# Optimization experiments

Hardware: AMD Instinct MI355X
Metric: run time of the kernel (lower is better)

## Reference

```python
import jax, jax.numpy as jnp
import numpy as np

EPS = 1e-5

def rmsnorm(x, w):
    var = jnp.mean(x * x, axis=-1, keepdims=True)
    return x * jax.lax.rsqrt(var + EPS) * w

def apply_rope(x, cos, sin):
    # x: [B, S, H, D], cos/sin: [S, D//2]; llama-style complex rotation over pairs
    B, S, H, D = x.shape
    xr = x.reshape(B, S, H, D // 2, 2)
    x0, x1 = xr[..., 0], xr[..., 1]
    c = cos[None, :, None, :]
    s = sin[None, :, None, :]
    o0 = x0 * c - x1 * s
    o1 = x0 * s + x1 * c
    return jnp.stack([o0, o1], axis=-1).reshape(B, S, H, D)

def setup_inputs() -> dict:
    key = jax.random.key(0)
    ks = jax.random.split(key, 8)
    B, S, dim = 2, 2048, 2048
    H, nope, rope = 16, 128, 64
    q_lr, kv_lr = 1536, 512
    hd = nope + rope
    x = jax.random.normal(ks[0], (B, S, dim), jnp.float32)
    wd_q = jax.random.normal(ks[1], (dim, q_lr), jnp.float32) * (dim ** -0.5)
    wu_q = jax.random.normal(ks[2], (q_lr, H * hd), jnp.float32) * (q_lr ** -0.5)
    q_norm_w = jnp.ones((q_lr,), jnp.float32)
    wd_kv = jax.random.normal(ks[3], (dim, kv_lr + rope), jnp.float32) * (dim ** -0.5)
    wu_kv = jax.random.normal(ks[4], (kv_lr, H * 2 * nope), jnp.float32) * (kv_lr ** -0.5)
    kv_norm_w = jnp.ones((kv_lr,), jnp.float32)
    wo = jax.random.normal(ks[5], (H * nope, dim), jnp.float32) * ((H * nope) ** -0.5)
    pos = jnp.arange(S, dtype=jnp.float32)
    inv_freq = 1.0 / (10000.0 ** (jnp.arange(0, rope, 2, dtype=jnp.float32) / rope))
    ang = pos[:, None] * inv_freq[None, :]  # [S, rope//2]
    return {"x": x, "wd_q": wd_q, "wu_q": wu_q, "q_norm_w": q_norm_w,
            "wd_kv": wd_kv, "wu_kv": wu_kv, "kv_norm_w": kv_norm_w, "wo": wo,
            "cos": jnp.cos(ang), "sin": jnp.sin(ang), "start_pos": 0}

def reference(x, wd_q, wu_q, q_norm_w, wd_kv, wu_kv, kv_norm_w, wo, cos, sin, start_pos):
    B, S, dim = x.shape
    H, nope, rope = 16, 128, 64
    kv_lr = 512
    hd = nope + rope
    # low-rank Q projection + RMSNorm
    cq = x @ wd_q
    xq = rmsnorm(cq, q_norm_w) @ wu_q
    xq = xq.reshape(B, S, H, hd)
    xq_nope, xq_rope = xq[..., :nope], xq[..., nope:]
    # low-rank KV projection
    kvd = x @ wd_kv
    ckv, xk_rope = kvd[..., :kv_lr], kvd[..., kv_lr:]
    xk_rope = xk_rope.reshape(B, S, 1, rope)
    kvu = (rmsnorm(ckv, kv_norm_w) @ wu_kv).reshape(B, S, H, 2 * nope)
    xk_nope, xv = kvu[..., :nope], kvu[..., nope:]
    # partial RoPE
    xq_rope = apply_rope(xq_rope, cos, sin)
    xk_rope = apply_rope(xk_rope, cos, sin)
    xk_rope = jnp.broadcast_to(xk_rope, (B, S, H, rope))
    q = jnp.concatenate([xq_nope, xq_rope], axis=-1)  # [B,S,H,192]
    k = jnp.concatenate([xk_nope, xk_rope], axis=-1)
    # causal SDPA
    scale = 1.0 / jnp.sqrt(jnp.float32(hd))
    scores = jnp.einsum('bqhd,bkhd->bhqk', q, k) * scale
    mask = jnp.tril(jnp.ones((S, S), bool))
    scores = jnp.where(mask[None, None], scores, jnp.finfo(scores.dtype).min)
    attn = jax.nn.softmax(scores, axis=-1)
    out = jnp.einsum('bhqk,bkhd->bqhd', attn, xv).reshape(B, S, H * nope)
    return out @ wo
```

## Files before the change

### kernel.cpp

```cpp
#include <hip/hip_runtime.h>
#include <hip/hip_bf16.h>

#define S_LEN 2048
#define NHEAD 16
#define NOPE 128
#define ROPE 64
#define HD 192

typedef unsigned short ushort_t;
typedef __attribute__((ext_vector_type(8))) short short8;
typedef __attribute__((ext_vector_type(4))) float f32x4;

#define AS1 __attribute__((address_space(1)))
#define AS3 __attribute__((address_space(3)))

__device__ __forceinline__ unsigned short f2bf(float f) {
  unsigned int u = __float_as_uint(f);
  return (unsigned short)((u + 0x7FFFu + ((u >> 16) & 1u)) >> 16);
}

__global__ __launch_bounds__(256) void prep_k(const float* __restrict__ x, ushort_t* __restrict__ xb,
                                              const float* __restrict__ wd_q, ushort_t* __restrict__ wdqt,
                                              const float* __restrict__ wd_kv, ushort_t* __restrict__ wdkvt,
                                              const float* __restrict__ wu_q, ushort_t* __restrict__ wuqt,
                                              const float* __restrict__ wu_kv, ushort_t* __restrict__ wukvt,
                                              const float* __restrict__ wo, ushort_t* __restrict__ wot) {
  int id = blockIdx.x;
  if (id < 4096) {
    const int i = id * 256 + threadIdx.x;
    const float4 v0 = *(const float4*)&x[(size_t)i * 8];
    const float4 v1 = *(const float4*)&x[(size_t)i * 8 + 4];
    union { uint4 u; ushort_t s[8]; } pk;
    pk.s[0] = f2bf(v0.x); pk.s[1] = f2bf(v0.y); pk.s[2] = f2bf(v0.z); pk.s[3] = f2bf(v0.w);
    pk.s[4] = f2bf(v1.x); pk.s[5] = f2bf(v1.y); pk.s[6] = f2bf(v1.z); pk.s[7] = f2bf(v1.w);
    *(uint4*)&xb[(size_t)i * 8] = pk.u;
    return;
  }
  id -= 4096;
  const float* B; ushort_t* Bt; int K, N, gx;
  if (id < 3072)               { B = wd_q;  Bt = wdqt;  K = 2048; N = 1536; gx = 48;  }
  else if ((id -= 3072) < 1280){ B = wd_kv; Bt = wdkvt; K = 2048; N = 576;  gx = 20;  }
  else if ((id -= 1280) < 4608){ B = wu_q;  Bt = wuqt;  K = 1536; N = 3072; gx = 96;  }
  else if ((id -= 4608) < 2048){ B = wu_kv; Bt = wukvt; K = 512;  N = 4096; gx = 128; }
  else { id -= 2048;             B = wo;    Bt = wot;   K = 2048; N = 2048; gx = 64;  }
  __shared__ float tile[32][33];
  const int tx = threadIdx.x & 31, ty = threadIdx.x >> 5;
  const int n0 = (id % gx) * 32, k0 = (id / gx) * 32;
  if (n0 >= N) {
#pragma unroll
    for (int r = 0; r < 4; ++r)
      Bt[(size_t)(n0 + ty + 8 * r) * K + k0 + tx] = 0;
    return;
  }
#pragma unroll
  for (int r = 0; r < 4; ++r)
    tile[ty + 8 * r][tx] = B[(size_t)(k0 + ty + 8 * r) * N + n0 + tx];
  __syncthreads();
#pragma unroll
  for (int r = 0; r < 4; ++r)
    Bt[(size_t)(n0 + ty + 8 * r) * K + k0 + tx] = f2bf(tile[tx][ty + 8 * r]);
}

template<int EPI>
__global__ __launch_bounds__(512, 4) void mfma_gemm(const ushort_t* __restrict__ A,
                                                 const ushort_t* __restrict__ Bt,
                                                 float* __restrict__ C,
                                                 int M, int N, int K, int ldc,
                                                 ushort_t* __restrict__ kb16o,
                                                 ushort_t* __restrict__ vto,
                                                 float* __restrict__ C2,
                                                 const float* __restrict__ cosb,
                                                 const float* __restrict__ sinb) {
  __shared__ ushort_t As[2][128 * 32];
  __shared__ ushort_t Bs[2][128 * 32];
  const int tid = threadIdx.x;
  const int lane = tid & 63;
  const int wave = tid >> 6;
  const int wm = wave & 3, wn = wave >> 2;

  unsigned bxu = blockIdx.x, byu = blockIdx.y;
  {
    const unsigned gx = gridDim.x;
    const unsigned nwg = gx * gridDim.y;
    if ((nwg & 7u) == 0u) {
      unsigned flat = byu * gx + bxu;
      const unsigned cpx = nwg >> 3;
      flat = (flat & 7u) * cpx + (flat >> 3);
      bxu = flat % gx; byu = flat / gx;
    }
  }
  const int m0 = byu * 128, n0 = bxu * 128;
  const int l15 = lane & 15, quad = lane >> 4;

  f32x4 acc[2][4] = {};

  const int ma0 = tid >> 2;
  const int scol = (((tid & 3) ^ ((tid >> 3) & 3)) << 3);
  const int rsw = (l15 >> 1) & 3;

  typedef AS3 ushort_t lds_us;
  lds_us* AsL = (lds_us*)As;
  lds_us* BsL = (lds_us*)Bs;
  const int wbase = wave * 512;

  auto issue = [&](int k0, int buf) {
    __builtin_amdgcn_global_load_lds(
        (const AS1 void*)&A[(size_t)(m0 + ma0) * K + k0 + scol],
        (AS3 void*)(AsL + buf * 4096 + wbase), 16, 0, 0);
    __builtin_amdgcn_global_load_lds(
        (const AS1 void*)&Bt[(size_t)(n0 + ma0) * K + k0 + scol],
        (AS3 void*)(BsL + buf * 4096 + wbase), 16, 0, 0);
  };

  const int nk = K >> 5;
  issue(0, 0);
  __builtin_amdgcn_sched_barrier(0);

  for (int ks = 0; ks < nk; ++ks) {
    const int buf = ks & 1;
    const bool more = (ks + 1 < nk);
    if (more) {
      issue((ks + 1) << 5, buf ^ 1);
      __builtin_amdgcn_sched_barrier(0);
      asm volatile("s_waitcnt vmcnt(2)" ::: "memory");
    } else {
      asm volatile("s_waitcnt vmcnt(0)" ::: "memory");
    }
    __builtin_amdgcn_s_barrier();
    __builtin_amdgcn_sched_barrier(0);

    short8 af[2], bf[4];
#pragma unroll
    for (int i = 0; i < 2; ++i)
      af[i] = *(const short8*)&As[buf][(wm * 32 + i * 16 + l15) * 32 + ((quad ^ rsw) << 3)];
#pragma unroll
    for (int j = 0; j < 4; ++j)
      bf[j] = *(const short8*)&Bs[buf][(wn * 64 + j * 16 + l15) * 32 + ((quad ^ rsw) << 3)];
    __builtin_amdgcn_s_setprio(1);
#pragma unroll
    for (int i = 0; i < 2; ++i)
#pragma unroll
      for (int j = 0; j < 4; ++j)
        acc[i][j] = __builtin_amdgcn_mfma_f32_16x16x32_bf16(af[i], bf[j], acc[i][j], 0, 0, 0);
    __builtin_amdgcn_s_setprio(0);
    __builtin_amdgcn_s_barrier();
    __builtin_amdgcn_sched_barrier(0);
  }

  if constexpr (EPI == 0) {
#pragma unroll
    for (int i = 0; i < 2; ++i)
#pragma unroll
      for (int r = 0; r < 4; ++r) {
        const size_t rg = (size_t)(m0 + wm * 32 + i * 16 + quad * 4 + r);
#pragma unroll
        for (int j = 0; j < 4; ++j)
          C[rg * ldc + n0 + wn * 64 + j * 16 + l15] = acc[i][j][r];
      }
  } else if constexpr (EPI == 1) {
    const int h = n0 >> 8;
    const bool is_v = (n0 >> 7) & 1;
    if (!is_v) {
#pragma unroll
      for (int i = 0; i < 2; ++i)
#pragma unroll
        for (int r = 0; r < 4; ++r) {
          const size_t rg = (size_t)(m0 + wm * 32 + i * 16 + quad * 4 + r);
#pragma unroll
          for (int j = 0; j < 4; ++j)
            kb16o[rg * 2048 + h * 128 + wn * 64 + j * 16 + l15] = f2bf(acc[i][j][r]);
        }
    } else {
      __shared__ __align__(16) ushort_t trb[64 * 136];
      const int bb = m0 >> 11;
      const int m0loc = m0 & 2047;
      ushort_t* vbase = vto + ((size_t)(bb * NHEAD + h) * 128) * 2048;
#pragma unroll
      for (int vh = 0; vh < 2; ++vh) {
        if (wn == vh) {
#pragma unroll
          for (int i = 0; i < 2; ++i)
#pragma unroll
            for (int r = 0; r < 4; ++r) {
              const int tloc = wm * 32 + i * 16 + quad * 4 + r;
#pragma unroll
              for (int j = 0; j < 4; ++j)
                trb[(j * 16 + l15) * 136 + tloc] = f2bf(acc[i][j][r]);
            }
        }
        __syncthreads();
#pragma unroll
        for (int it = 0; it < 2; ++it) {
          const int u = tid + (it << 9);
          const int vdl = u >> 4, tc = u & 15;
          *(uint4*)&vbase[(size_t)(vh * 64 + vdl) * 2048 + m0loc + tc * 8] =
              *(const uint4*)&trb[vdl * 136 + tc * 8];
        }
        __syncthreads();
      }
    }
  } else if constexpr (EPI == 2) {
    float* Cd;
    int ldd, nc;
    if (n0 < 1536) { Cd = C;  ldd = 1536; nc = n0; }
    else           { Cd = C2; ldd = 640;  nc = n0 - 1536; }
#pragma unroll
    for (int i = 0; i < 2; ++i)
#pragma unroll
      for (int r = 0; r < 4; ++r) {
        const size_t rg = (size_t)(m0 + wm * 32 + i * 16 + quad * 4 + r);
#pragma unroll
        for (int j = 0; j < 4; ++j)
          Cd[rg * ldd + nc + wn * 64 + j * 16 + l15] = acc[i][j][r];
      }
  } else {
    const float qscale = 0.07216878364870323f;
#pragma unroll
    for (int i = 0; i < 2; ++i)
#pragma unroll
      for (int r = 0; r < 4; ++r) {
        const int rg = m0 + wm * 32 + i * 16 + quad * 4 + r;
        const int sp = rg & (S_LEN - 1);
#pragma unroll
        for (int j = 0; j < 4; ++j) {
          const int col = n0 + wn * 64 + j * 16 + l15;
          float val = acc[i][j][r] * qscale;
          const float pr = __shfl_xor(val, 1);
          const int dd = col % HD;
          float o = val;
          if (dd >= NOPE) {
            const int d = (dd - NOPE) >> 1;
            const float cc = cosb[sp * 32 + d];
            const float sn = sinb[sp * 32 + d];
            o = (lane & 1) ? (pr * sn + val * cc) : (val * cc - pr * sn);
          }
          kb16o[(size_t)rg * 3072 + col] = f2bf(o);
        }
      }
  }
}

__global__ __launch_bounds__(256) void rmsnorm2_k(const float* __restrict__ cq,
                                                  ushort_t* __restrict__ cqn,
                                                  const float* __restrict__ qw,
                                                  const float* __restrict__ kvd,
                                                  ushort_t* __restrict__ ckvn,
                                                  const float* __restrict__ kvw,
                                                  ushort_t* __restrict__ krope16,
                                                  const float* __restrict__ cosb,
                                                  const float* __restrict__ sinb) {
  const bool is_q = blockIdx.x < 4096;
  const int row = blockIdx.x & 4095;
  const int tid = threadIdx.x;
  const float* ip = is_q ? cq + (size_t)row * 1536 : kvd + (size_t)row * 640;
  ushort_t* op = is_q ? cqn + (size_t)row * 1536 : ckvn + (size_t)row * 512;
  const float* w = is_q ? qw : kvw;
  const int L = is_q ? 1536 : 512;
  const int nper = L >> 8;
  float r[6];
  float ss = 0.f;
  for (int j = 0; j < nper; ++j) {
    r[j] = ip[tid + (j << 8)];
    ss += r[j] * r[j];
  }
  for (int off = 32; off; off >>= 1) ss += __shfl_down(ss, off);
  __shared__ float wsum[4];
  __shared__ float scale_s;
  if ((tid & 63) == 0) wsum[tid >> 6] = ss;
  __syncthreads();
  if (tid == 0) {
    float t = wsum[0] + wsum[1] + wsum[2] + wsum[3];
    scale_s = rsqrtf(t / (float)L + 1e-5f);
  }
  __syncthreads();
  const float sc = scale_s;
  for (int j = 0; j < nper; ++j)
    op[tid + (j << 8)] = f2bf(r[j] * sc * w[tid + (j << 8)]);
  if (!is_q && tid < 32) {
    const int d = tid;
    const int s = row & (S_LEN - 1);
    const float c = cosb[s * 32 + d];
    const float sn = sinb[s * 32 + d];
    const float* kb = kvd + (size_t)row * 640 + 512;
    const float y0 = kb[2 * d], y1 = kb[2 * d + 1];
    union { unsigned int u; ushort_t s2[2]; } pk;
    pk.s2[0] = f2bf(y0 * c - y1 * sn);
    pk.s2[1] = f2bf(y0 * sn + y1 * c);
    *(unsigned int*)&krope16[(size_t)row * 64 + 2 * d] = pk.u;
  }
}

#define QT 128
#define KC 64
__global__ __launch_bounds__(512, 4) void attn_k(const ushort_t* __restrict__ q16,
                                                 const ushort_t* __restrict__ kb16,
                                                 const ushort_t* __restrict__ vT,
                                                 const ushort_t* __restrict__ krope16,
                                                 ushort_t* __restrict__ outp) {
  const int bx = blockIdx.x;
  const int g = bx & 31;
  const int s = bx >> 5;
  const int tile = (s < 8) ? s : 23 - s;
  const int b = g >> 4, h = g & 15;
  const int q0 = tile * QT;
  const int tid = threadIdx.x;
  const int lane = tid & 63;
  const int wq = tid >> 6;
  const int l15 = lane & 15, quad = lane >> 4;

  __shared__ __align__(16) ushort_t Kn[64 * 128];
  __shared__ __align__(16) ushort_t Kr[64 * 64];
  __shared__ __align__(16) ushort_t Vt[2][128 * 64];
  __shared__ __align__(16) ushort_t Pb[8][16 * 72];

  const int qbase = q0 + wq * 16;
  const size_t growq = (size_t)b * S_LEN + qbase;
  const ushort_t* vTh = vT + ((size_t)(b * NHEAD + h) * 128) * 2048;
  const size_t bbase = (size_t)b * S_LEN;

  typedef AS3 ushort_t lds_us;
  lds_us* KnL = (lds_us*)Kn;
  lds_us* KrL = (lds_us*)Kr;
  lds_us* VtL = (lds_us*)Vt;
  const int wbase = wq * 512;

  auto issueK = [&](int c) {
    const size_t growk = bbase + (size_t)c * KC;
#pragma unroll
    for (int it = 0; it < 2; ++it) {
      const int u = tid + (it << 9);
      const int key = u >> 4, sl = u & 15;
      const int ss = sl ^ (key & 7);
      __builtin_amdgcn_global_load_lds(
          (const AS1 void*)&kb16[(growk + key) * 2048 + h * 128 + ss * 8],
          (AS3 void*)(KnL + wbase + it * 4096), 16, 0, 0);
    }
    {
      const int u = tid;
      const int key = u >> 3, sl = u & 7;
      const int ss = sl ^ (key & 7);
      __builtin_amdgcn_global_load_lds(
          (const AS1 void*)&krope16[(growk + key) * 64 + ss * 8],
          (AS3 void*)(KrL + wbase), 16, 0, 0);
    }
  };
  auto issueV = [&](int c, int buf) {
    const int j0 = c * KC;
#pragma unroll
    for (int it = 0; it < 2; ++it) {
      const int u = tid + (it << 9);
      const int vd = u >> 3, sl = u & 7;
      const int ss = sl ^ (vd & 7);
      __builtin_amdgcn_global_load_lds(
          (const AS1 void*)&vTh[(size_t)vd * 2048 + j0 + ss * 8],
          (AS3 void*)(VtL + buf * 8192 + wbase + it * 4096), 16, 0, 0);
    }
  };

  issueK(0);
  issueV(0, 0);
  __builtin_amdgcn_sched_barrier(0);

  short8 qf[6];
#pragma unroll
  for (int ks = 0; ks < 6; ++ks)
    qf[ks] = *(const short8*)&q16[(growq + l15) * 3072 + h * HD + ks * 32 + quad * 8];

  f32x4 oacc[8] = {};
  float mrow[4], lrow[4];
  int q_r[4];
#pragma unroll
  for (int r = 0; r < 4; ++r) {
    mrow[r] = -1e30f; lrow[r] = 0.f;
    q_r[r] = qbase + quad * 4 + r;
  }

  const int nchunk = (q0 + QT) / KC;

  asm volatile("s_waitcnt vmcnt(2)" ::: "memory");
  __builtin_amdgcn_s_barrier();
  __builtin_amdgcn_sched_barrier(0);

  for (int c = 0; c < nchunk; ++c) {
    const int j0 = c * KC;
    const bool more = (c + 1 < nchunk);
    const int buf = c & 1;
    const bool skipw = (j0 > qbase + 15);

    f32x4 sacc[4] = {};
    if (!skipw) {
      __builtin_amdgcn_s_setprio(1);
#pragma unroll
      for (int ks = 0; ks < 6; ++ks) {
        short8 kf[4];
        if (ks < 4) {
#pragma unroll
          for (int kt = 0; kt < 4; ++kt)
            kf[kt] = *(const short8*)&Kn[(kt * 16 + l15) * 128 + (((ks * 4 + quad) ^ (l15 & 7)) << 3)];
        } else {
#pragma unroll
          for (int kt = 0; kt < 4; ++kt)
            kf[kt] = *(const short8*)&Kr[(kt * 16 + l15) * 64 + ((((ks - 4) * 4 + quad) ^ (l15 & 7)) << 3)];
        }
#pragma unroll
        for (int kt = 0; kt < 4; ++kt)
          sacc[kt] = __builtin_amdgcn_mfma_f32_16x16x32_bf16(qf[ks], kf[kt], sacc[kt], 0, 0, 0);
      }
      __builtin_amdgcn_s_setprio(0);
    }

    __builtin_amdgcn_s_barrier();
    if (more) issueK(c + 1);
    __builtin_amdgcn_sched_barrier(0);

    if (!skipw) {
      if (j0 + KC - 1 > qbase) {
#pragma unroll
        for (int kt = 0; kt < 4; ++kt) {
          const int key = j0 + kt * 16 + l15;
#pragma unroll
          for (int r = 0; r < 4; ++r)
            sacc[kt][r] = (key <= q_r[r]) ? sacc[kt][r] : -1e30f;
        }
      }
      float pmax[4];
#pragma unroll
      for (int r = 0; r < 4; ++r) {
        float mx = fmaxf(fmaxf(sacc[0][r], sacc[1][r]),
                         fmaxf(sacc[2][r], sacc[3][r]));
        mx = fmaxf(mx, __shfl_xor(mx, 1));
        mx = fmaxf(mx, __shfl_xor(mx, 2));
        mx = fmaxf(mx, __shfl_xor(mx, 4));
        mx = fmaxf(mx, __shfl_xor(mx, 8));
        pmax[r] = mx;
      }
      bool need = false;
#pragma unroll
      for (int r = 0; r < 4; ++r)
        need = need || (pmax[r] > mrow[r] + 8.0f);
      const bool upd = __any(need);
      float alpha[4];
      if (upd) {
#pragma unroll
        for (int r = 0; r < 4; ++r) {
          const float mn = fmaxf(mrow[r], pmax[r]);
          alpha[r] = __expf(mrow[r] - mn);
          mrow[r] = mn;
        }
      }
#pragma unroll
      for (int kt = 0; kt < 4; ++kt)
#pragma unroll
        for (int r = 0; r < 4; ++r)
          sacc[kt][r] = __expf(sacc[kt][r] - mrow[r]);
#pragma unroll
      for (int r = 0; r < 4; ++r) {
        float rs = sacc[0][r] + sacc[1][r] + sacc[2][r] + sacc[3][r];
        rs += __shfl_xor(rs, 1);
        rs += __shfl_xor(rs, 2);
        rs += __shfl_xor(rs, 4);
        rs += __shfl_xor(rs, 8);
        lrow[r] = upd ? lrow[r] * alpha[r] + rs : lrow[r] + rs;
      }
#pragma unroll
      for (int kt = 0; kt < 4; ++kt)
#pragma unroll
        for (int r = 0; r < 4; ++r)
          Pb[wq][(quad * 4 + r) * 72 + kt * 16 + l15] = f2bf(sacc[kt][r]);
      if (upd) {
#pragma unroll
        for (int nt = 0; nt < 8; ++nt)
#pragma unroll
          for (int r = 0; r < 4; ++r)
            oacc[nt][r] *= alpha[r];
      }
    }

    if (more) asm volatile("s_waitcnt vmcnt(3)" ::: "memory");
    else      asm volatile("s_waitcnt vmcnt(0)" ::: "memory");
    __builtin_amdgcn_s_barrier();
    __builtin_amdgcn_sched_barrier(0);

    if (!skipw) {
      __builtin_amdgcn_s_setprio(1);
#pragma unroll
      for (int st = 0; st < 2; ++st) {
        const short8 pf = *(const short8*)&Pb[wq][l15 * 72 + st * 32 + quad * 8];
#pragma unroll
        for (int nt = 0; nt < 8; ++nt) {
          const short8 vf = *(const short8*)&Vt[buf][(nt * 16 + l15) * 64 + (((st * 4 + quad) ^ (l15 & 7)) << 3)];
          oacc[nt] = __builtin_amdgcn_mfma_f32_16x16x32_bf16(pf, vf, oacc[nt], 0, 0, 0);
        }
      }
      __builtin_amdgcn_s_setprio(0);
    }

    if (more) {
      issueV(c + 1, buf ^ 1);
      __builtin_amdgcn_sched_barrier(0);
      asm volatile("s_waitcnt vmcnt(2)" ::: "memory");
      __builtin_amdgcn_s_barrier();
      __builtin_amdgcn_sched_barrier(0);
    }
  }

#pragma unroll
  for (int r = 0; r < 4; ++r) {
    const float inv = 1.0f / lrow[r];
    const size_t orow = growq + quad * 4 + r;
#pragma unroll
    for (int nt = 0; nt < 8; ++nt)
      outp[orow * 2048 + h * 128 + nt * 16 + l15] = f2bf(oacc[nt][r] * inv);
  }
}

extern "C" void kernel_launch(void* const* d_in, const int* in_sizes, int n_in,
                              void* d_out, int out_size, void* d_ws, size_t ws_size,
                              hipStream_t stream) {
  const float* x        = (const float*)d_in[0];
  const float* wd_q     = (const float*)d_in[1];
  const float* wu_q     = (const float*)d_in[2];
  const float* q_norm_w = (const float*)d_in[3];
  const float* wd_kv    = (const float*)d_in[4];
  const float* wu_kv    = (const float*)d_in[5];
  const float* kv_norm_w= (const float*)d_in[6];
  const float* wo       = (const float*)d_in[7];
  const float* cosb     = (const float*)d_in[8];
  const float* sinb     = (const float*)d_in[9];
  float* out = (float*)d_out;

  char* ws = (char*)d_ws;
  float*    cq    = (float*)(ws + 0);
  ushort_t* q16   = (ushort_t*)(ws + 0);
  ushort_t* kb16  = (ushort_t*)(ws + 50331648);
  ushort_t* vT    = (ushort_t*)(ws + 67108864);
  ushort_t* xb    = (ushort_t*)(ws + 83886080);
  ushort_t* cqn   = (ushort_t*)(ws + 117440512);
  float*    kvd   = (float*)(ws + 130023424);
  ushort_t* ckvn  = (ushort_t*)(ws + 140509184);
  ushort_t* aoutb = (ushort_t*)(ws + 130023424);
  ushort_t* krope16 = (ushort_t*)(ws + 146800640);
  ushort_t* wdqt  = (ushort_t*)(ws + 147849216);
  ushort_t* wdkvt = (ushort_t*)(ws + 154140672);
  ushort_t* wuqt  = (ushort_t*)(ws + 156762112);
  ushort_t* wukvt = (ushort_t*)(ws + 166199296);
  ushort_t* wot   = (ushort_t*)(ws + 170393600);

  const int M = 2 * S_LEN;
  dim3 blk(256);
  dim3 blk512(512);

  prep_k<<<19200, blk, 0, stream>>>(x, xb, wd_q, wdqt, wd_kv, wdkvt,
                                    wu_q, wuqt, wu_kv, wukvt, wo, wot);

  mfma_gemm<2><<<dim3(2176 / 128, M / 128), blk512, 0, stream>>>(
      xb, wdqt, cq, M, 2176, 2048, 1536, nullptr, nullptr, kvd, nullptr, nullptr);
  rmsnorm2_k<<<2 * M, 256, 0, stream>>>(cq, cqn, q_norm_w, kvd, ckvn, kv_norm_w,
                                        krope16, cosb, sinb);
  mfma_gemm<3><<<dim3(3072 / 128, M / 128), blk512, 0, stream>>>(
      cqn, wuqt, nullptr, M, 3072, 1536, 0, q16, nullptr, nullptr, cosb, sinb);
  mfma_gemm<1><<<dim3(4096 / 128, M / 128), blk512, 0, stream>>>(
      ckvn, wukvt, nullptr, M, 4096, 512, 0, kb16, vT, nullptr, nullptr, nullptr);
  attn_k<<<2 * NHEAD * (S_LEN / QT), 512, 0, stream>>>(q16, kb16, vT, krope16, aoutb);
  mfma_gemm<0><<<dim3(2048 / 128, M / 128), blk512, 0, stream>>>(
      aoutb, wot, out, M, 2048, 2048, 2048, nullptr, nullptr, nullptr, nullptr, nullptr);
}
```

Measured before the change: 444.1 us.

## Split attention key range across two wave groups per block and merge results

The attention block grows to 1024 threads as two groups of eight waves. Each group processes half of the causal key chunks with its own double-buffered K, K-rope and V tiles in shared memory. At the end the partial outputs and running max/sum are combined through shared memory using softmax rescaling. This aims to shorten each block's serial chunk loop and balance causal work, at the cost of much larger LDS use (likely one block per CU) and an extra merge step.

```diff
diff --git a/kernel.cpp b/kernel.cpp
--- a/kernel.cpp
+++ b/kernel.cpp
@@ -292,11 +292,11 @@
 
 #define QT 128
 #define KC 64
-__global__ __launch_bounds__(512, 4) void attn_k(const ushort_t* __restrict__ q16,
-                                                 const ushort_t* __restrict__ kb16,
-                                                 const ushort_t* __restrict__ vT,
-                                                 const ushort_t* __restrict__ krope16,
-                                                 ushort_t* __restrict__ outp) {
+__global__ __launch_bounds__(1024, 4) void attn_k(const ushort_t* __restrict__ q16,
+                                                  const ushort_t* __restrict__ kb16,
+                                                  const ushort_t* __restrict__ vT,
+                                                  const ushort_t* __restrict__ krope16,
+                                                  ushort_t* __restrict__ outp) {
   const int bx = blockIdx.x;
   const int g = bx & 31;
   const int s = bx >> 5;
@@ -305,15 +305,18 @@
   const int q0 = tile * QT;
   const int tid = threadIdx.x;
   const int lane = tid & 63;
-  const int wq = tid >> 6;
+  const int wv = tid >> 6;
+  const int wg = wv >> 3;
+  const int wq8 = wv & 7;
+  const int gtid = tid & 511;
   const int l15 = lane & 15, quad = lane >> 4;
 
-  __shared__ __align__(16) ushort_t Kn[64 * 128];
-  __shared__ __align__(16) ushort_t Kr[64 * 64];
-  __shared__ __align__(16) ushort_t Vt[2][128 * 64];
-  __shared__ __align__(16) ushort_t Pb[8][16 * 72];
-
-  const int qbase = q0 + wq * 16;
+  __shared__ __align__(16) ushort_t Kn[2][64 * 128];
+  __shared__ __align__(16) ushort_t Kr[2][64 * 64];
+  __shared__ __align__(16) ushort_t Vt[2][2][128 * 64];
+  __shared__ __align__(16) ushort_t Pb[16][16 * 72];
+
+  const int qbase = q0 + wq8 * 16;
   const size_t growq = (size_t)b * S_LEN + qbase;
   const ushort_t* vTh = vT + ((size_t)(b * NHEAD + h) * 128) * 2048;
   const size_t bbase = (size_t)b * S_LEN;
@@ -322,43 +325,46 @@
   lds_us* KnL = (lds_us*)Kn;
   lds_us* KrL = (lds_us*)Kr;
   lds_us* VtL = (lds_us*)Vt;
-  const int wbase = wq * 512;
 
   auto issueK = [&](int c) {
     const size_t growk = bbase + (size_t)c * KC;
 #pragma unroll
     for (int it = 0; it < 2; ++it) {
-      const int u = tid + (it << 9);
+      const int u = gtid + (it << 9);
       const int key = u >> 4, sl = u & 15;
       const int ss = sl ^ (key & 7);
       __builtin_amdgcn_global_load_lds(
           (const AS1 void*)&kb16[(growk + key) * 2048 + h * 128 + ss * 8],
-          (AS3 void*)(KnL + wbase + it * 4096), 16, 0, 0);
+          (AS3 void*)(KnL + wg * 8192 + it * 4096 + wq8 * 512), 16, 0, 0);
     }
     {
-      const int u = tid;
+      const int u = gtid;
       const int key = u >> 3, sl = u & 7;
       const int ss = sl ^ (key & 7);
       __builtin_amdgcn_global_load_lds(
           (const AS1 void*)&krope16[(growk + key) * 64 + ss * 8],
-          (AS3 void*)(KrL + wbase), 16, 0, 0);
+          (AS3 void*)(KrL + wg * 4096 + wq8 * 512), 16, 0, 0);
     }
   };
   auto issueV = [&](int c, int buf) {
     const int j0 = c * KC;
 #pragma unroll
     for (int it = 0; it < 2; ++it) {
-      const int u = tid + (it << 9);
+      const int u = gtid + (it << 9);
       const int vd = u >> 3, sl = u & 7;
       const int ss = sl ^ (vd & 7);
       __builtin_amdgcn_global_load_lds(
           (const AS1 void*)&vTh[(size_t)vd * 2048 + j0 + ss * 8],
-          (AS3 void*)(VtL + buf * 8192 + wbase + it * 4096), 16, 0, 0);
+          (AS3 void*)(VtL + (wg * 2 + buf) * 8192 + it * 4096 + wq8 * 512), 16, 0, 0);
     }
   };
 
-  issueK(0);
-  issueV(0, 0);
+  const int nchunk = (q0 + QT) / KC;
+  const int half = nchunk >> 1;
+  const int cbase = wg * half;
+
+  issueK(cbase);
+  issueV(cbase, 0);
   __builtin_amdgcn_sched_barrier(0);
 
   short8 qf[6];
@@ -375,16 +381,15 @@
     q_r[r] = qbase + quad * 4 + r;
   }
 
-  const int nchunk = (q0 + QT) / KC;
-
   asm volatile("s_waitcnt vmcnt(2)" ::: "memory");
   __builtin_amdgcn_s_barrier();
   __builtin_amdgcn_sched_barrier(0);
 
-  for (int c = 0; c < nchunk; ++c) {
+  for (int cl = 0; cl < half; ++cl) {
+    const int c = cbase + cl;
     const int j0 = c * KC;
-    const bool more = (c + 1 < nchunk);
-    const int buf = c & 1;
+    const bool more = (cl + 1 < half);
+    const int buf = cl & 1;
     const bool skipw = (j0 > qbase + 15);
 
     f32x4 sacc[4] = {};
@@ -396,11 +401,11 @@
         if (ks < 4) {
 #pragma unroll
           for (int kt = 0; kt < 4; ++kt)
-            kf[kt] = *(const short8*)&Kn[(kt * 16 + l15) * 128 + (((ks * 4 + quad) ^ (l15 & 7)) << 3)];
+            kf[kt] = *(const short8*)&Kn[wg][(kt * 16 + l15) * 128 + (((ks * 4 + quad) ^ (l15 & 7)) << 3)];
         } else {
 #pragma unroll
           for (int kt = 0; kt < 4; ++kt)
-            kf[kt] = *(const short8*)&Kr[(kt * 16 + l15) * 64 + ((((ks - 4) * 4 + quad) ^ (l15 & 7)) << 3)];
+            kf[kt] = *(const short8*)&Kr[wg][(kt * 16 + l15) * 64 + ((((ks - 4) * 4 + quad) ^ (l15 & 7)) << 3)];
         }
 #pragma unroll
         for (int kt = 0; kt < 4; ++kt)
@@ -466,7 +471,7 @@
       for (int kt = 0; kt < 4; ++kt)
 #pragma unroll
         for (int r = 0; r < 4; ++r)
-          Pb[wq][(quad * 4 + r) * 72 + kt * 16 + l15] = f2bf(sacc[kt][r]);
+          Pb[wv][(quad * 4 + r) * 72 + kt * 16 + l15] = f2bf(sacc[kt][r]);
       if (upd) {
 #pragma unroll
         for (int nt = 0; nt < 8; ++nt)
@@ -485,10 +490,10 @@
       __builtin_amdgcn_s_setprio(1);
 #pragma unroll
       for (int st = 0; st < 2; ++st) {
-        const short8 pf = *(const short8*)&Pb[wq][l15 * 72 + st * 32 + quad * 8];
+        const short8 pf = *(const short8*)&Pb[wv][l15 * 72 + st * 32 + quad * 8];
 #pragma unroll
         for (int nt = 0; nt < 8; ++nt) {
-          const short8 vf = *(const short8*)&Vt[buf][(nt * 16 + l15) * 64 + (((st * 4 + quad) ^ (l15 & 7)) << 3)];
+          const short8 vf = *(const short8*)&Vt[wg][buf][(nt * 16 + l15) * 64 + (((st * 4 + quad) ^ (l15 & 7)) << 3)];
           oacc[nt] = __builtin_amdgcn_mfma_f32_16x16x32_bf16(pf, vf, oacc[nt], 0, 0, 0);
         }
       }
@@ -504,13 +509,41 @@
     }
   }
 
-#pragma unroll
-  for (int r = 0; r < 4; ++r) {
-    const float inv = 1.0f / lrow[r];
-    const size_t orow = growq + quad * 4 + r;
+  __builtin_amdgcn_s_barrier();
+  float* Ocmb = (float*)&Vt[0][0][0];
+  float* Mlb  = (float*)&Kn[0][0];
+  if (wg == 1) {
 #pragma unroll
     for (int nt = 0; nt < 8; ++nt)
-      outp[orow * 2048 + h * 128 + nt * 16 + l15] = f2bf(oacc[nt][r] * inv);
+#pragma unroll
+      for (int r = 0; r < 4; ++r)
+        Ocmb[(size_t)(wq8 * 16 + quad * 4 + r) * 128 + nt * 16 + l15] = oacc[nt][r];
+    if (l15 == 0) {
+#pragma unroll
+      for (int r = 0; r < 4; ++r) {
+        Mlb[(wq8 * 16 + quad * 4 + r) * 2 + 0] = mrow[r];
+        Mlb[(wq8 * 16 + quad * 4 + r) * 2 + 1] = lrow[r];
+      }
+    }
+  }
+  __builtin_amdgcn_s_barrier();
+  if (wg == 0) {
+#pragma unroll
+    for (int r = 0; r < 4; ++r) {
+      const int row = wq8 * 16 + quad * 4 + r;
+      const float m1 = Mlb[row * 2 + 0];
+      const float l1 = Mlb[row * 2 + 1];
+      const float mx = fmaxf(mrow[r], m1);
+      const float w0 = __expf(mrow[r] - mx);
+      const float w1 = __expf(m1 - mx);
+      const float inv = 1.0f / (lrow[r] * w0 + l1 * w1);
+      const size_t orow = growq + quad * 4 + r;
+#pragma unroll
+      for (int nt = 0; nt < 8; ++nt) {
+        const float o = oacc[nt][r] * w0 + Ocmb[(size_t)row * 128 + nt * 16 + l15] * w1;
+        outp[orow * 2048 + h * 128 + nt * 16 + l15] = f2bf(o * inv);
+      }
+    }
   }
 }
 
@@ -561,7 +594,7 @@
       cqn, wuqt, nullptr, M, 3072, 1536, 0, q16, nullptr, nullptr, cosb, sinb);
   mfma_gemm<1><<<dim3(4096 / 128, M / 128), blk512, 0, stream>>>(
       ckvn, wukvt, nullptr, M, 4096, 512, 0, kb16, vT, nullptr, nullptr, nullptr);
-  attn_k<<<2 * NHEAD * (S_LEN / QT), 512, 0, stream>>>(q16, kb16, vT, krope16, aoutb);
+  attn_k<<<2 * NHEAD * (S_LEN / QT), 1024, 0, stream>>>(q16, kb16, vT, krope16, aoutb);
   mfma_gemm<0><<<dim3(2048 / 128, M / 128), blk512, 0, stream>>>(
       aoutb, wot, out, M, 2048, 2048, 2048, nullptr, nullptr, nullptr, nullptr, nullptr);
 }
```

New measurement: 444.5 us. No clear change (+0.1%).
